# Kernel optimization log

Measured on AMD Instinct MI355X. Metric: run time of the kernel, lower is better.

The kernel has to match this reference:

```python
import jax, jax.numpy as jnp
import numpy as np

BATCH, IN, HID, OMID, OUT = 8192, 64, 1024, 128, 1
MAX_ITER = 8
EPS = 1e-3


def setup_inputs() -> dict:
    key = jax.random.key(0)
    ks = jax.random.split(key, 32)
    s_in, s_h = 1.0 / np.sqrt(IN), 1.0 / np.sqrt(HID)
    d = {"x": jax.random.normal(ks[0], (BATCH, IN), jnp.float32)}
    names = ["i", "f", "c", "o"]
    for j, n in enumerate(names):
        d[f"Wx{n}"] = jax.random.uniform(ks[1 + 4 * j], (HID, IN), jnp.float32, -s_in, s_in)
        d[f"bx{n}"] = jax.random.uniform(ks[2 + 4 * j], (HID,), jnp.float32, -s_in, s_in)
        d[f"Wh{n}"] = jax.random.uniform(ks[3 + 4 * j], (HID, HID), jnp.float32, -s_h, s_h)
        d[f"bh{n}"] = jax.random.uniform(ks[4 + 4 * j], (HID,), jnp.float32, -s_h, s_h)
    d["W_halt"] = jax.random.uniform(ks[20], (1, HID), jnp.float32, -s_h, s_h)
    d["b_halt"] = jax.random.uniform(ks[21], (1,), jnp.float32, -s_h, s_h)
    d["W1"] = jax.random.uniform(ks[22], (OMID, HID), jnp.float32, -s_h, s_h)
    d["b1"] = jax.random.uniform(ks[23], (OMID,), jnp.float32, -s_h, s_h)
    s_m = 1.0 / np.sqrt(OMID)
    d["W2"] = jax.random.uniform(ks[24], (OUT, OMID), jnp.float32, -s_m, s_m)
    d["b2"] = jax.random.uniform(ks[25], (OUT,), jnp.float32, -s_m, s_m)
    return d


def _act_forward(x, Wxi, bxi, Whi, bhi, Wxf, bxf, Whf, bhf, Wxc, bxc, Whc, bhc,
                 Wxo, bxo, Who, bho, W_halt, b_halt, W1, b1, W2, b2):
    B = x.shape[0]
    state0 = jnp.zeros((B, HID), x.dtype)
    cell0 = jnp.zeros((B, HID), x.dtype)
    p0 = jnp.zeros((B,), x.dtype)
    active0 = jnp.ones((B,), bool)

    def step(carry, t):
        state, cell, p_sum, active = carry
        # four LSTM-style gates (computed dense; masked update == torch's gather/scatter)
        i_g = jax.nn.sigmoid(x @ Wxi.T + bxi + state @ Whi.T + bhi)
        f_g = jax.nn.sigmoid(x @ Wxf.T + bxf + state @ Whf.T + bhf)
        c_g = jnp.tanh(x @ Wxc.T + bxc + state @ Whc.T + bhc)
        o_g = jax.nn.sigmoid(x @ Wxo.T + bxo + state @ Who.T + bho)
        am = active[:, None]
        cell = jnp.where(am, f_g * cell + i_g * c_g, cell)
        state = jnp.where(am, o_g * jnp.tanh(cell), state)
        out = jax.nn.sigmoid(jax.nn.relu(state @ W1.T + b1) @ W2.T + b2)  # (B, OUT)
        h = jax.nn.sigmoid(state @ W_halt.T + b_halt)[:, 0]               # (B,)
        p_new = p_sum + h
        last = t == MAX_ITER - 1
        finished = active & ((p_new >= 1.0 - EPS) | last)
        halt_rec = jnp.where(finished, 1.0 - p_sum, jnp.where(active, h, 0.0))
        p_sum = jnp.where(finished, 1.0, jnp.where(active, p_new, p_sum))
        out_rec = jnp.where(am, out, 0.0)
        active = active & ~finished
        return (state, cell, p_sum, active), (out_rec, halt_rec)

    _, (outs, halts) = jax.lax.scan(step, (state0, cell0, p0, active0), jnp.arange(MAX_ITER))
    # outs: (T, B, OUT), halts: (T, B); final = sum_t out_t * p_halt_t
    return jnp.einsum("tbo,tb->bo", outs, halts)


def reference(x, Wxi, bxi, Whi, bhi, Wxf, bxf, Whf, bhf, Wxc, bxc, Whc, bhc,
              Wxo, bxo, Who, bho, W_halt, b_halt, W1, b1, W2, b2):
    return _act_forward(x, Wxi, bxi, Whi, bhi, Wxf, bxf, Whf, bhf, Wxc, bxc, Whc, bhc,
                        Wxo, bxo, Who, bho, W_halt, b_halt, W1, b1, W2, b2)
```

## Files before the change

kernel.cpp:

```cpp
#include <hip/hip_runtime.h>
#include <hip/hip_bf16.h>

#define BATCH 8192
#define IN_DIM 64
#define HID 1024
#define KTOT 1088
#define NGATES 4096
#define OMID 128
#define NP 256
#define MAX_ITER 8

#define TM 128
#define TN 128
#define TK 64
#define TAILB 64

typedef __attribute__((ext_vector_type(8))) short short8;
typedef __attribute__((ext_vector_type(4))) float float4v;

__device__ __forceinline__ float bf2f(short s) {
    union { float f; unsigned u; } v; v.u = ((unsigned)(unsigned short)s) << 16; return v.f;
}
__device__ __forceinline__ short f2bf(float f) {
    union { float f; unsigned u; } v; v.f = f;
    unsigned r = v.u + 0x7fff + ((v.u >> 16) & 1);
    return (short)(r >> 16);
}
__device__ __forceinline__ float sigmoidf_(float x) {
    float xc = fminf(fmaxf(x, -30.f), 30.f);
    return 1.f / (1.f + __expf(-xc));
}
__device__ __forceinline__ float tanhf_(float x) {
    float xc = fminf(fmaxf(x, -15.f), 15.f);
    float e = __expf(2.f * xc);
    return (e - 1.f) / (e + 1.f);
}
__device__ __forceinline__ int aload(const int* p) {
    return __hip_atomic_load((int*)p, __ATOMIC_RELAXED, __HIP_MEMORY_SCOPE_AGENT);
}
__device__ __forceinline__ void astore(int* p, int v) {
    __hip_atomic_store(p, v, __ATOMIC_RELAXED, __HIP_MEMORY_SCOPE_AGENT);
}

__device__ __forceinline__ void gbar(int* bar, int phase, int tid) {
    __syncthreads();
    if (tid == 0) {
        __threadfence();
        __hip_atomic_fetch_add(bar, 1, __ATOMIC_ACQ_REL, __HIP_MEMORY_SCOPE_AGENT);
        while (aload(bar) < TAILB * phase)
            __builtin_amdgcn_s_sleep(8);
        __threadfence();
    }
    __syncthreads();
}

__device__ __forceinline__ void gates_tile(
    short* As, short* Bs, int tid,
    const short* __restrict__ A, const short* __restrict__ B,
    const float* __restrict__ bias_g, int K,
    float* __restrict__ cell, short* __restrict__ Aout,
    const int* __restrict__ ridx, int n_act, int m0, int bx)
{
    const int wave = tid >> 6, lane = tid & 63;
    const int wm = wave & 1, wn = wave >> 1;
    const int colq = lane & 15, q = lane >> 4;
    const int lrow8 = lane >> 3;
    const int lk    = (((lane & 7) ^ lrow8) * 8);
    const int n0 = bx * TN;

    int aoff[4][2], boff[4][2];
#pragma unroll
    for (int i = 0; i < 4; ++i) {
        const int Ra = wm * 64 + i * 16 + colq;
        const int Rb = wn * 64 + i * 16 + colq;
#pragma unroll
        for (int c2 = 0; c2 < 2; ++c2) {
            const int C = q + 4 * c2;
            aoff[i][c2] = Ra * TK + ((C ^ (Ra & 7)) << 3);
            boff[i][c2] = Rb * TK + ((C ^ (Rb & 7)) << 3);
        }
    }

    float4v acc[4][4];
#pragma unroll
    for (int i = 0; i < 4; ++i)
#pragma unroll
        for (int j = 0; j < 4; ++j) acc[i][j] = (float4v)0.f;

    const short* ga[4];
    const short* gb[4];
#pragma unroll
    for (int it = 0; it < 4; ++it) {
        const int rr = (wave * 4 + it) * 8;
        ga[it] = A + (size_t)ridx[m0 + rr + lrow8] * KTOT + lk;
        gb[it] = B + (size_t)(n0 + rr + lrow8) * KTOT + lk;
    }

    for (int k0 = 0; k0 < K; k0 += TK) {
#pragma unroll
        for (int it = 0; it < 4; ++it) {
            const int rr = (wave * 4 + it) * 8;
            __builtin_amdgcn_global_load_lds(
                (const __attribute__((address_space(1))) void*)ga[it],
                (__attribute__((address_space(3))) void*)(As + rr * TK), 16, 0, 0);
            __builtin_amdgcn_global_load_lds(
                (const __attribute__((address_space(1))) void*)gb[it],
                (__attribute__((address_space(3))) void*)(Bs + rr * TK), 16, 0, 0);
            ga[it] += TK; gb[it] += TK;
        }
        __syncthreads();
#pragma unroll
        for (int c2 = 0; c2 < 2; ++c2) {
            short8 af[4], bf[4];
#pragma unroll
            for (int i = 0; i < 4; ++i) {
                af[i] = *(const short8*)(As + aoff[i][c2]);
                bf[i] = *(const short8*)(Bs + boff[i][c2]);
            }
#pragma unroll
            for (int i = 0; i < 4; ++i)
#pragma unroll
                for (int j = 0; j < 4; ++j)
                    acc[i][j] = __builtin_amdgcn_mfma_f32_16x16x32_bf16(af[i], bf[j], acc[i][j], 0, 0, 0);
        }
        __syncthreads();
    }

    const int G = bx * 2 + wn;
    const int h = G * 16 + colq;
    const float bi  = bias_g[G * 64 +  0 + colq];
    const float bff = bias_g[G * 64 + 16 + colq];
    const float bc  = bias_g[G * 64 + 32 + colq];
    const float bo  = bias_g[G * 64 + 48 + colq];
#pragma unroll
    for (int i = 0; i < 4; ++i) {
        const int pbase = m0 + wm * 64 + i * 16 + q * 4;
#pragma unroll
        for (int r = 0; r < 4; ++r) {
            const int pos = pbase + r;
            if (pos < n_act) {
                const int row = ridx[pos];
                const float ig = sigmoidf_(acc[i][0][r] + bi);
                const float fg = sigmoidf_(acc[i][1][r] + bff);
                const float cg = tanhf_(acc[i][2][r] + bc);
                const float og = sigmoidf_(acc[i][3][r] + bo);
                const size_t ci = (size_t)row * HID + h;
                const float c = fg * cell[ci] + ig * cg;
                cell[ci] = c;
                Aout[(size_t)row * KTOT + h] = f2bf(og * tanhf_(c));
            }
        }
    }
    __syncthreads();
}

__device__ __forceinline__ void midfin_tile(
    short* As, short* Bs, int tid,
    const short* __restrict__ Anew, const short* __restrict__ P,
    const float* __restrict__ bias_p, const float* __restrict__ W_halt,
    const float* __restrict__ W2, const float* __restrict__ b2,
    float* __restrict__ outp, float* __restrict__ p_sum,
    const int* __restrict__ rprev, int* __restrict__ rnext,
    int* __restrict__ cnt, int t, int m0, int n_act)
{
    const int wave = tid >> 6, lane = tid & 63;
    const int wm = wave & 1, wn = wave >> 1;
    const int colq = lane & 15, q = lane >> 4;
    const int lrow8 = lane >> 3;
    const int lk    = (((lane & 7) ^ lrow8) * 8);

    float4v acc[4][4];
#pragma unroll
    for (int i = 0; i < 4; ++i)
#pragma unroll
        for (int j = 0; j < 4; ++j) acc[i][j] = (float4v)0.f;

    const short* ga[4];
    const short* gb[4];
#pragma unroll
    for (int it = 0; it < 4; ++it) {
        const int rr = (wave * 4 + it) * 8;
        ga[it] = Anew + (size_t)rprev[m0 + rr + lrow8] * KTOT + lk;
        gb[it] = P + (size_t)(rr + lrow8) * HID + lk;
    }
    int aoff[4][2], boff[4][2];
#pragma unroll
    for (int i = 0; i < 4; ++i) {
        const int Ra = wm * 64 + i * 16 + colq;
        const int Rb = wn * 64 + i * 16 + colq;
#pragma unroll
        for (int c2 = 0; c2 < 2; ++c2) {
            const int C = q + 4 * c2;
            aoff[i][c2] = Ra * TK + ((C ^ (Ra & 7)) << 3);
            boff[i][c2] = Rb * TK + ((C ^ (Rb & 7)) << 3);
        }
    }

    for (int k0 = 0; k0 < HID; k0 += TK) {
#pragma unroll
        for (int it = 0; it < 4; ++it) {
            const int rr = (wave * 4 + it) * 8;
            __builtin_amdgcn_global_load_lds(
                (const __attribute__((address_space(1))) void*)ga[it],
                (__attribute__((address_space(3))) void*)(As + rr * TK), 16, 0, 0);
            __builtin_amdgcn_global_load_lds(
                (const __attribute__((address_space(1))) void*)gb[it],
                (__attribute__((address_space(3))) void*)(Bs + rr * TK), 16, 0, 0);
            ga[it] += TK; gb[it] += TK;
        }
        __syncthreads();
#pragma unroll
        for (int c2 = 0; c2 < 2; ++c2) {
            short8 af[4], bf[4];
#pragma unroll
            for (int i = 0; i < 4; ++i) {
                af[i] = *(const short8*)(As + aoff[i][c2]);
                bf[i] = *(const short8*)(Bs + boff[i][c2]);
            }
#pragma unroll
            for (int i = 0; i < 4; ++i)
#pragma unroll
                for (int j = 0; j < 4; ++j)
                    acc[i][j] = __builtin_amdgcn_mfma_f32_16x16x32_bf16(af[i], bf[j], acc[i][j], 0, 0, 0);
        }
        __syncthreads();
    }

    float* red  = (float*)As;
    float* hbuf = ((float*)As) + 256;

    for (int s = 0; s < 32; ++s) {
        const int lr = wave * 32 + s;
        const int row = rprev[m0 + lr];
        const short* Ar = Anew + (size_t)row * KTOT + lane * 16;
        const short8 v0 = *(const short8*)Ar;
        const short8 v1 = *(const short8*)(Ar + 8);
        const float* Wh = W_halt + lane * 16;
        float hv = 0.f;
#pragma unroll
        for (int e = 0; e < 8; ++e) hv += bf2f(v0[e]) * Wh[e];
#pragma unroll
        for (int e = 0; e < 8; ++e) hv += bf2f(v1[e]) * Wh[8 + e];
#pragma unroll
        for (int o = 32; o > 0; o >>= 1) hv += __shfl_down(hv, o);
        if (lane == 0) hbuf[lr] = hv;
    }

    float pr[4][4];
#pragma unroll
    for (int i = 0; i < 4; ++i)
#pragma unroll
        for (int r = 0; r < 4; ++r) pr[i][r] = 0.f;
#pragma unroll
    for (int j = 0; j < 4; ++j) {
        const int col = wn * 64 + j * 16 + colq;
        const float b = bias_p[col];
        const float w2 = W2[col];
#pragma unroll
        for (int i = 0; i < 4; ++i)
#pragma unroll
            for (int r = 0; r < 4; ++r)
                pr[i][r] += fmaxf(acc[i][j][r] + b, 0.f) * w2;
    }
#pragma unroll
    for (int i = 0; i < 4; ++i)
#pragma unroll
        for (int r = 0; r < 4; ++r) {
            float v = pr[i][r];
            v += __shfl_down(v, 8, 16);
            v += __shfl_down(v, 4, 16);
            v += __shfl_down(v, 2, 16);
            v += __shfl_down(v, 1, 16);
            if (colq == 0)
                red[((((wn * 2) + wm) * 4 + i) * 4 + q) * 4 + r] = v;
        }
    __syncthreads();

    if (tid < TM) {
        const int pos = m0 + tid;
        if (pos < n_act) {
            const int lwm = tid >> 6, i = (tid >> 4) & 3, lq = (tid >> 2) & 3, r = tid & 3;
            const float odot = red[((lwm * 4 + i) * 4 + lq) * 4 + r]
                             + red[(((2 + lwm) * 4 + i) * 4 + lq) * 4 + r];
            const int row = rprev[pos];
            const float ov = sigmoidf_(odot + b2[0]);
            const float h  = sigmoidf_(hbuf[tid] + bias_p[OMID]);
            const float ps = p_sum[row];
            const float pn = ps + h;
            const bool fin = (pn >= 1.f - 1e-3f) || (t == MAX_ITER - 1);
            const float halt = fin ? (1.f - ps) : h;
            outp[row] += ov * halt;
            p_sum[row] = fin ? 1.f : pn;
            if (!fin) {
                const int d = atomicAdd(&cnt[t + 1], 1);
                astore(&rnext[d], row);
            }
        }
    }
    __syncthreads();
}

__global__ __launch_bounds__(256) void gates_k(
    const short* __restrict__ A, const short* __restrict__ B,
    const float* __restrict__ bias_g, int K,
    float* __restrict__ cell, short* __restrict__ Aout,
    const int* __restrict__ ridx, const int* __restrict__ cnt, int t)
{
    __shared__ short As[TM * TK];
    __shared__ short Bs[TN * TK];
    const int n_act = cnt[t];
    for (int by = blockIdx.y; by * TM < n_act; by += gridDim.y)
        gates_tile(As, Bs, threadIdx.x, A, B, bias_g, K, cell, Aout,
                   ridx, n_act, by * TM, blockIdx.x);
}

__global__ __launch_bounds__(256) void midfin_k(
    const short* __restrict__ Anew, const short* __restrict__ P,
    const float* __restrict__ bias_p, const float* __restrict__ W_halt,
    const float* __restrict__ W2, const float* __restrict__ b2,
    float* __restrict__ outp, float* __restrict__ p_sum,
    const int* __restrict__ rprev, int* __restrict__ rnext,
    int* __restrict__ cnt, int t)
{
    __shared__ short As[TM * TK];
    __shared__ short Bs[TN * TK];
    const int n_act = cnt[t];
    for (int tile = blockIdx.x; tile * TM < n_act; tile += gridDim.x)
        midfin_tile(As, Bs, threadIdx.x, Anew, P, bias_p, W_halt, W2, b2,
                    outp, p_sum, rprev, rnext, cnt, t, tile * TM, n_act);
}

__global__ __launch_bounds__(256) void tail_k(
    const short* __restrict__ Wg, const float* __restrict__ bias_g,
    const short* __restrict__ P, const float* __restrict__ bias_p,
    const float* __restrict__ W_halt, const float* __restrict__ W2,
    const float* __restrict__ b2,
    short* __restrict__ A0, short* __restrict__ A1,
    float* __restrict__ cell, float* __restrict__ outp,
    float* __restrict__ p_sum,
    int* __restrict__ ridx0, int* __restrict__ ridx1,
    int* __restrict__ cnt, int* __restrict__ bar)
{
    __shared__ short As[TM * TK];
    __shared__ short Bs[TN * TK];
    const int tid = threadIdx.x;
    int phase = 0;
    int t = 2;
    while (true) {
        short* Anew = (t & 1) ? A0 : A1;
        const int* rprev = (t & 1) ? ridx1 : ridx0;
        int* rnext = (t & 1) ? ridx0 : ridx1;
        const int n = aload(&cnt[t]);
        for (int tile = blockIdx.x; tile * TM < n; tile += gridDim.x)
            midfin_tile(As, Bs, tid, Anew, P, bias_p, W_halt, W2, b2,
                        outp, p_sum, rprev, rnext, cnt, t, tile * TM, n);
        if (t == MAX_ITER - 1) break;
        ++phase; gbar(bar, phase, tid);
        const int n1 = aload(&cnt[t + 1]);
        if (n1 == 0) break;
        {
            short* Aot = (t & 1) ? A1 : A0;
            const int ntiles = ((n1 + TM - 1) / TM) * (NGATES / TN);
            for (int e = blockIdx.x; e < ntiles; e += gridDim.x)
                gates_tile(As, Bs, tid, Anew, Wg, bias_g, KTOT, cell, Aot,
                           rnext, n1, (e >> 5) * TM, e & 31);
        }
        ++phase; gbar(bar, phase, tid);
        ++t;
    }
}

#define SETUP_INIT  (BATCH * KTOT)
#define SETUP_WG    (NGATES * KTOT)
#define SETUP_P     (NP * HID)
#define SETUP_TOT   (SETUP_INIT + SETUP_WG + SETUP_P)
__global__ __launch_bounds__(256) void setup_k(
    const float* __restrict__ x,
    const float* __restrict__ Whi, const float* __restrict__ Whf,
    const float* __restrict__ Whc, const float* __restrict__ Who,
    const float* __restrict__ Wxi, const float* __restrict__ Wxf,
    const float* __restrict__ Wxc, const float* __restrict__ Wxo,
    const float* __restrict__ bxi, const float* __restrict__ bhi,
    const float* __restrict__ bxf, const float* __restrict__ bhf,
    const float* __restrict__ bxc, const float* __restrict__ bhc,
    const float* __restrict__ bxo, const float* __restrict__ bho,
    const float* __restrict__ W1, const float* __restrict__ b1,
    const float* __restrict__ W_halt, const float* __restrict__ b_halt,
    short* __restrict__ A0, short* __restrict__ A1,
    float* __restrict__ cell, float* __restrict__ p_sum,
    int* __restrict__ ridx0, int* __restrict__ ridx1, int* __restrict__ cnt,
    int* __restrict__ bar, float* __restrict__ outp,
    short* __restrict__ Wg, float* __restrict__ bias_g,
    short* __restrict__ P, float* __restrict__ bias_p)
{
    int idx = blockIdx.x * 256 + threadIdx.x;
    if (idx < SETUP_INIT) {
        const int row = idx / KTOT, k = idx - row * KTOT;
        const short v = (k < HID) ? (short)0 : f2bf(x[row * IN_DIM + (k - HID)]);
        A0[idx] = v;
        A1[idx] = v;
        if (k < HID) cell[(size_t)row * HID + k] = 0.f;
        if (k == 0) {
            p_sum[row] = 0.f;
            outp[row] = 0.f;
            ridx0[row] = row;
            ridx1[row] = 0;
        }
        if (row == 0 && k <= MAX_ITER) cnt[k] = (k == 0) ? BATCH : 0;
        if (row == 1 && k == 0) bar[0] = 0;
        return;
    }
    idx -= SETUP_INIT;
    if (idx < SETUP_WG) {
        const int n = idx / KTOT, k = idx - n * KTOT;
        const int G = n >> 6, g = (n >> 4) & 3, q = n & 15;
        const int h = G * 16 + q;
        const float* Wh = (g == 0) ? Whi : (g == 1) ? Whf : (g == 2) ? Whc : Who;
        const float* Wx = (g == 0) ? Wxi : (g == 1) ? Wxf : (g == 2) ? Wxc : Wxo;
        const float v = (k < HID) ? Wh[h * HID + k] : Wx[h * IN_DIM + (k - HID)];
        Wg[idx] = f2bf(v);
        if (k == 0) {
            const float* bx = (g == 0) ? bxi : (g == 1) ? bxf : (g == 2) ? bxc : bxo;
            const float* bh = (g == 0) ? bhi : (g == 1) ? bhf : (g == 2) ? bhc : bho;
            bias_g[n] = bx[h] + bh[h];
        }
        return;
    }
    idx -= SETUP_WG;
    if (idx < SETUP_P) {
        const int n = idx >> 10, k = idx & 1023;
        const float v = (n < OMID) ? W1[n * HID + k] : (n == OMID ? W_halt[k] : 0.f);
        P[idx] = f2bf(v);
        if (k == 0) bias_p[n] = (n < OMID) ? b1[n] : (n == OMID ? b_halt[0] : 0.f);
    }
}

extern "C" void kernel_launch(void* const* d_in, const int* in_sizes, int n_in,
                              void* d_out, int out_size, void* d_ws, size_t ws_size,
                              hipStream_t stream) {
    const float* x    = (const float*)d_in[0];
    const float* Wxi  = (const float*)d_in[1];
    const float* bxi  = (const float*)d_in[2];
    const float* Whi  = (const float*)d_in[3];
    const float* bhi  = (const float*)d_in[4];
    const float* Wxf  = (const float*)d_in[5];
    const float* bxf  = (const float*)d_in[6];
    const float* Whf  = (const float*)d_in[7];
    const float* bhf  = (const float*)d_in[8];
    const float* Wxc  = (const float*)d_in[9];
    const float* bxc  = (const float*)d_in[10];
    const float* Whc  = (const float*)d_in[11];
    const float* bhc  = (const float*)d_in[12];
    const float* Wxo  = (const float*)d_in[13];
    const float* bxo  = (const float*)d_in[14];
    const float* Who  = (const float*)d_in[15];
    const float* bho  = (const float*)d_in[16];
    const float* W_halt = (const float*)d_in[17];
    const float* b_halt = (const float*)d_in[18];
    const float* W1   = (const float*)d_in[19];
    const float* b1   = (const float*)d_in[20];
    const float* W2   = (const float*)d_in[21];
    const float* b2   = (const float*)d_in[22];

    char* p = (char*)d_ws;
    auto carve = [&](size_t bytes) { char* r = p; p += (bytes + 255) & ~(size_t)255; return r; };
    short* A0     = (short*)carve((size_t)BATCH * KTOT * 2);
    short* A1     = (short*)carve((size_t)BATCH * KTOT * 2);
    short* Wg     = (short*)carve((size_t)NGATES * KTOT * 2);
    float* bias_g = (float*)carve((size_t)NGATES * 4);
    short* P      = (short*)carve((size_t)NP * HID * 2);
    float* bias_p = (float*)carve((size_t)NP * 4);
    float* cell   = (float*)carve((size_t)BATCH * HID * 4);
    float* p_sum  = (float*)carve((size_t)BATCH * 4);
    int*   ridx0  = (int*)carve((size_t)BATCH * 4);
    int*   ridx1  = (int*)carve((size_t)BATCH * 4);
    int*   cnt    = (int*)carve((size_t)(MAX_ITER + 1) * 4);
    int*   bar    = (int*)carve(256);
    float* outp   = (float*)d_out;

    setup_k<<<(SETUP_TOT + 255) / 256, 256, 0, stream>>>(
        x, Whi, Whf, Whc, Who, Wxi, Wxf, Wxc, Wxo,
        bxi, bhi, bxf, bhf, bxc, bhc, bxo, bho,
        W1, b1, W_halt, b_halt,
        A0, A1, cell, p_sum, ridx0, ridx1, cnt, bar, outp,
        Wg, bias_g, P, bias_p);

    gates_k<<<dim3(NGATES / TN, 32), 256, 0, stream>>>(
        A0 + HID, Wg + HID, bias_g, IN_DIM, cell, A1, ridx0, cnt, 0);
    midfin_k<<<64, 256, 0, stream>>>(
        A1, P, bias_p, W_halt, W2, b2, outp, p_sum, ridx0, ridx1, cnt, 0);
    gates_k<<<dim3(NGATES / TN, 32), 256, 0, stream>>>(
        A1, Wg, bias_g, KTOT, cell, A0, ridx1, cnt, 1);
    midfin_k<<<64, 256, 0, stream>>>(
        A0, P, bias_p, W_halt, W2, b2, outp, p_sum, ridx1, ridx0, cnt, 1);
    gates_k<<<dim3(NGATES / TN, 32), 256, 0, stream>>>(
        A0, Wg, bias_g, KTOT, cell, A1, ridx0, cnt, 2);
    tail_k<<<TAILB, 256, 0, stream>>>(
        Wg, bias_g, P, bias_p, W_halt, W2, b2,
        A0, A1, cell, outp, p_sum, ridx0, ridx1, cnt, bar);
}
```

Baseline: 496.4 us.

## Load gate GEMM operands directly from global memory into registers, bypassing LDS

The gates GEMM tile no longer stages A and B tiles through shared memory with global_load_lds and two barriers per K step. Each wave now loads its MFMA fragments straight from global memory (L2/L1), and the trailing block barrier is dropped. This removes LDS traffic and synchronisation, but each tile's data is fetched redundantly by several waves, and the per-lane loads are strided rather than coalesced. That can raise cache and memory pressure.

Measured after the change: 730.2 us. 47.1% more time.

```diff
diff --git a/kernel.cpp b/kernel.cpp
--- a/kernel.cpp
+++ b/kernel.cpp
@@ -55,8 +55,9 @@
 }
 
 __device__ __forceinline__ void gates_tile(
-    short* As, short* Bs, int tid,
-    const short* __restrict__ A, const short* __restrict__ B,
+    int tid,
+    const short* __restrict__ A,
+    const short* __restrict__ B,
     const float* __restrict__ bias_g, int K,
     float* __restrict__ cell, short* __restrict__ Aout,
     const int* __restrict__ ridx, int n_act, int m0, int bx)
@@ -64,21 +65,13 @@
     const int wave = tid >> 6, lane = tid & 63;
     const int wm = wave & 1, wn = wave >> 1;
     const int colq = lane & 15, q = lane >> 4;
-    const int lrow8 = lane >> 3;
-    const int lk    = (((lane & 7) ^ lrow8) * 8);
-    const int n0 = bx * TN;
-
-    int aoff[4][2], boff[4][2];
+
+    const short* pa[4];
+    const short* pb[4];
 #pragma unroll
     for (int i = 0; i < 4; ++i) {
-        const int Ra = wm * 64 + i * 16 + colq;
-        const int Rb = wn * 64 + i * 16 + colq;
-#pragma unroll
-        for (int c2 = 0; c2 < 2; ++c2) {
-            const int C = q + 4 * c2;
-            aoff[i][c2] = Ra * TK + ((C ^ (Ra & 7)) << 3);
-            boff[i][c2] = Rb * TK + ((C ^ (Rb & 7)) << 3);
-        }
+        pa[i] = A + (size_t)ridx[m0 + wm * 64 + i * 16 + colq] * KTOT + q * 8;
+        pb[i] = B + (size_t)(bx * TN + wn * 64 + i * 16 + colq) * KTOT + q * 8;
     }
 
     float4v acc[4][4];
@@ -87,43 +80,17 @@
 #pragma unroll
         for (int j = 0; j < 4; ++j) acc[i][j] = (float4v)0.f;
 
-    const short* ga[4];
-    const short* gb[4];
-#pragma unroll
-    for (int it = 0; it < 4; ++it) {
-        const int rr = (wave * 4 + it) * 8;
-        ga[it] = A + (size_t)ridx[m0 + rr + lrow8] * KTOT + lk;
-        gb[it] = B + (size_t)(n0 + rr + lrow8) * KTOT + lk;
-    }
-
-    for (int k0 = 0; k0 < K; k0 += TK) {
-#pragma unroll
-        for (int it = 0; it < 4; ++it) {
-            const int rr = (wave * 4 + it) * 8;
-            __builtin_amdgcn_global_load_lds(
-                (const __attribute__((address_space(1))) void*)ga[it],
-                (__attribute__((address_space(3))) void*)(As + rr * TK), 16, 0, 0);
-            __builtin_amdgcn_global_load_lds(
-                (const __attribute__((address_space(1))) void*)gb[it],
-                (__attribute__((address_space(3))) void*)(Bs + rr * TK), 16, 0, 0);
-            ga[it] += TK; gb[it] += TK;
-        }
-        __syncthreads();
-#pragma unroll
-        for (int c2 = 0; c2 < 2; ++c2) {
-            short8 af[4], bf[4];
-#pragma unroll
-            for (int i = 0; i < 4; ++i) {
-                af[i] = *(const short8*)(As + aoff[i][c2]);
-                bf[i] = *(const short8*)(Bs + boff[i][c2]);
-            }
-#pragma unroll
-            for (int i = 0; i < 4; ++i)
-#pragma unroll
-                for (int j = 0; j < 4; ++j)
-                    acc[i][j] = __builtin_amdgcn_mfma_f32_16x16x32_bf16(af[i], bf[j], acc[i][j], 0, 0, 0);
-        }
-        __syncthreads();
+    for (int k0 = 0; k0 < K; k0 += 32) {
+        short8 af[4], bf[4];
+#pragma unroll
+        for (int i = 0; i < 4; ++i) af[i] = *(const short8*)(pa[i] + k0);
+#pragma unroll
+        for (int j = 0; j < 4; ++j) bf[j] = *(const short8*)(pb[j] + k0);
+#pragma unroll
+        for (int i = 0; i < 4; ++i)
+#pragma unroll
+            for (int j = 0; j < 4; ++j)
+                acc[i][j] = __builtin_amdgcn_mfma_f32_16x16x32_bf16(af[i], bf[j], acc[i][j], 0, 0, 0);
     }
 
     const int G = bx * 2 + wn;
@@ -151,7 +118,6 @@
             }
         }
     }
-    __syncthreads();
 }
 
 __device__ __forceinline__ void midfin_tile(
@@ -306,11 +272,9 @@
     float* __restrict__ cell, short* __restrict__ Aout,
     const int* __restrict__ ridx, const int* __restrict__ cnt, int t)
 {
-    __shared__ short As[TM * TK];
-    __shared__ short Bs[TN * TK];
     const int n_act = cnt[t];
     for (int by = blockIdx.y; by * TM < n_act; by += gridDim.y)
-        gates_tile(As, Bs, threadIdx.x, A, B, bias_g, K, cell, Aout,
+        gates_tile(threadIdx.x, A, B, bias_g, K, cell, Aout,
                    ridx, n_act, by * TM, blockIdx.x);
 }
 
@@ -362,7 +326,7 @@
             short* Aot = (t & 1) ? A1 : A0;
             const int ntiles = ((n1 + TM - 1) / TM) * (NGATES / TN);
             for (int e = blockIdx.x; e < ntiles; e += gridDim.x)
-                gates_tile(As, Bs, tid, Anew, Wg, bias_g, KTOT, cell, Aot,
+                gates_tile(tid, Anew, Wg, bias_g, KTOT, cell, Aot,
                            rnext, n1, (e >> 5) * TM, e & 31);
         }
         ++phase; gbar(bar, phase, tid);
```

## Compute two M tiles per gates block to reuse each loaded B tile

Applied to the files above, without the earlier changes.

The gates GEMM kernel now has each block process two 128-row M tiles at once, sharing one loaded weight (B) tile between them, and the grid's y dimension is halved to match. This doubles the MFMA work per B load and cuts weight traffic through LDS and from global memory. In exchange the kernel needs twice the accumulator registers and more LDS, which limits it to 2 blocks per CU via launch bounds. When the second tile is inactive, its LDS buffer is still read, so it does wasted work on stale data. The old gates_tile is kept for the tail kernel.

New measurement: 457.7 us. -7.8%, faster.

```diff
diff --git a/kernel.cpp b/kernel.cpp
--- a/kernel.cpp
+++ b/kernel.cpp
@@ -13,6 +13,7 @@
 #define TM 128
 #define TN 128
 #define TK 64
+#define GYD 16
 #define TAILB 64
 
 typedef __attribute__((ext_vector_type(8))) short short8;
@@ -54,78 +55,13 @@
     __syncthreads();
 }
 
-__device__ __forceinline__ void gates_tile(
-    short* As, short* Bs, int tid,
-    const short* __restrict__ A, const short* __restrict__ B,
-    const float* __restrict__ bias_g, int K,
-    float* __restrict__ cell, short* __restrict__ Aout,
-    const int* __restrict__ ridx, int n_act, int m0, int bx)
-{
-    const int wave = tid >> 6, lane = tid & 63;
+__device__ __forceinline__ void gates_epilogue(
+    const float4v (&acc)[4][4], int m0, int bx, int wave, int lane,
+    const float* __restrict__ bias_g, float* __restrict__ cell,
+    short* __restrict__ Aout, const int* __restrict__ ridx, int n_act)
+{
     const int wm = wave & 1, wn = wave >> 1;
     const int colq = lane & 15, q = lane >> 4;
-    const int lrow8 = lane >> 3;
-    const int lk    = (((lane & 7) ^ lrow8) * 8);
-    const int n0 = bx * TN;
-
-    int aoff[4][2], boff[4][2];
-#pragma unroll
-    for (int i = 0; i < 4; ++i) {
-        const int Ra = wm * 64 + i * 16 + colq;
-        const int Rb = wn * 64 + i * 16 + colq;
-#pragma unroll
-        for (int c2 = 0; c2 < 2; ++c2) {
-            const int C = q + 4 * c2;
-            aoff[i][c2] = Ra * TK + ((C ^ (Ra & 7)) << 3);
-            boff[i][c2] = Rb * TK + ((C ^ (Rb & 7)) << 3);
-        }
-    }
-
-    float4v acc[4][4];
-#pragma unroll
-    for (int i = 0; i < 4; ++i)
-#pragma unroll
-        for (int j = 0; j < 4; ++j) acc[i][j] = (float4v)0.f;
-
-    const short* ga[4];
-    const short* gb[4];
-#pragma unroll
-    for (int it = 0; it < 4; ++it) {
-        const int rr = (wave * 4 + it) * 8;
-        ga[it] = A + (size_t)ridx[m0 + rr + lrow8] * KTOT + lk;
-        gb[it] = B + (size_t)(n0 + rr + lrow8) * KTOT + lk;
-    }
-
-    for (int k0 = 0; k0 < K; k0 += TK) {
-#pragma unroll
-        for (int it = 0; it < 4; ++it) {
-            const int rr = (wave * 4 + it) * 8;
-            __builtin_amdgcn_global_load_lds(
-                (const __attribute__((address_space(1))) void*)ga[it],
-                (__attribute__((address_space(3))) void*)(As + rr * TK), 16, 0, 0);
-            __builtin_amdgcn_global_load_lds(
-                (const __attribute__((address_space(1))) void*)gb[it],
-                (__attribute__((address_space(3))) void*)(Bs + rr * TK), 16, 0, 0);
-            ga[it] += TK; gb[it] += TK;
-        }
-        __syncthreads();
-#pragma unroll
-        for (int c2 = 0; c2 < 2; ++c2) {
-            short8 af[4], bf[4];
-#pragma unroll
-            for (int i = 0; i < 4; ++i) {
-                af[i] = *(const short8*)(As + aoff[i][c2]);
-                bf[i] = *(const short8*)(Bs + boff[i][c2]);
-            }
-#pragma unroll
-            for (int i = 0; i < 4; ++i)
-#pragma unroll
-                for (int j = 0; j < 4; ++j)
-                    acc[i][j] = __builtin_amdgcn_mfma_f32_16x16x32_bf16(af[i], bf[j], acc[i][j], 0, 0, 0);
-        }
-        __syncthreads();
-    }
-
     const int G = bx * 2 + wn;
     const int h = G * 16 + colq;
     const float bi  = bias_g[G * 64 +  0 + colq];
@@ -151,6 +87,178 @@
             }
         }
     }
+}
+
+__global__ __launch_bounds__(256, 2) void gates_k(
+    const short* __restrict__ A, const short* __restrict__ B,
+    const float* __restrict__ bias_g, int K,
+    float* __restrict__ cell, short* __restrict__ Aout,
+    const int* __restrict__ ridx, const int* __restrict__ cnt, int t)
+{
+    __shared__ short Bs[TN * TK];
+    __shared__ short As0[TM * TK];
+    __shared__ short As1[TM * TK];
+    const int n_act = cnt[t];
+    const int tid  = threadIdx.x;
+    const int wave = tid >> 6, lane = tid & 63;
+    const int wm = wave & 1, wn = wave >> 1;
+    const int colq = lane & 15, q = lane >> 4;
+    const int lrow8 = lane >> 3;
+    const int lk    = (((lane & 7) ^ lrow8) * 8);
+    const int n0 = blockIdx.x * TN;
+
+    int aoff[4][2], boff[4][2];
+#pragma unroll
+    for (int i = 0; i < 4; ++i) {
+        const int Ra = wm * 64 + i * 16 + colq;
+        const int Rb = wn * 64 + i * 16 + colq;
+#pragma unroll
+        for (int c2 = 0; c2 < 2; ++c2) {
+            const int C = q + 4 * c2;
+            aoff[i][c2] = Ra * TK + ((C ^ (Ra & 7)) << 3);
+            boff[i][c2] = Rb * TK + ((C ^ (Rb & 7)) << 3);
+        }
+    }
+
+    for (int by0 = blockIdx.y; by0 * TM < n_act; by0 += 2 * (int)gridDim.y) {
+        const int by1 = by0 + gridDim.y;
+        const bool dual = (by1 * TM < n_act);
+        const int m0 = by0 * TM, m1 = by1 * TM;
+
+        float4v acc0[4][4], acc1[4][4];
+#pragma unroll
+        for (int i = 0; i < 4; ++i)
+#pragma unroll
+            for (int j = 0; j < 4; ++j) { acc0[i][j] = (float4v)0.f; acc1[i][j] = (float4v)0.f; }
+
+        const short* ga0[4];
+        const short* ga1[4];
+        const short* gb[4];
+#pragma unroll
+        for (int it = 0; it < 4; ++it) {
+            const int rr = (wave * 4 + it) * 8;
+            ga0[it] = A + (size_t)ridx[m0 + rr + lrow8] * KTOT + lk;
+            ga1[it] = dual ? A + (size_t)ridx[m1 + rr + lrow8] * KTOT + lk : ga0[it];
+            gb[it]  = B + (size_t)(n0 + rr + lrow8) * KTOT + lk;
+        }
+
+        for (int k0 = 0; k0 < K; k0 += TK) {
+#pragma unroll
+            for (int it = 0; it < 4; ++it) {
+                const int rr = (wave * 4 + it) * 8;
+                __builtin_amdgcn_global_load_lds(
+                    (const __attribute__((address_space(1))) void*)gb[it],
+                    (__attribute__((address_space(3))) void*)(Bs + rr * TK), 16, 0, 0);
+                __builtin_amdgcn_global_load_lds(
+                    (const __attribute__((address_space(1))) void*)ga0[it],
+                    (__attribute__((address_space(3))) void*)(As0 + rr * TK), 16, 0, 0);
+                if (dual)
+                    __builtin_amdgcn_global_load_lds(
+                        (const __attribute__((address_space(1))) void*)ga1[it],
+                        (__attribute__((address_space(3))) void*)(As1 + rr * TK), 16, 0, 0);
+                ga0[it] += TK; ga1[it] += TK; gb[it] += TK;
+            }
+            __syncthreads();
+#pragma unroll
+            for (int c2 = 0; c2 < 2; ++c2) {
+                short8 bf[4], af0[4], af1[4];
+#pragma unroll
+                for (int i = 0; i < 4; ++i) {
+                    bf[i]  = *(const short8*)(Bs  + boff[i][c2]);
+                    af0[i] = *(const short8*)(As0 + aoff[i][c2]);
+                    af1[i] = *(const short8*)(As1 + aoff[i][c2]);
+                }
+#pragma unroll
+                for (int i = 0; i < 4; ++i)
+#pragma unroll
+                    for (int j = 0; j < 4; ++j) {
+                        acc0[i][j] = __builtin_amdgcn_mfma_f32_16x16x32_bf16(af0[i], bf[j], acc0[i][j], 0, 0, 0);
+                        acc1[i][j] = __builtin_amdgcn_mfma_f32_16x16x32_bf16(af1[i], bf[j], acc1[i][j], 0, 0, 0);
+                    }
+            }
+            __syncthreads();
+        }
+
+        gates_epilogue(acc0, m0, blockIdx.x, wave, lane, bias_g, cell, Aout, ridx, n_act);
+        if (dual)
+            gates_epilogue(acc1, m1, blockIdx.x, wave, lane, bias_g, cell, Aout, ridx, n_act);
+        __syncthreads();
+    }
+}
+
+__device__ __forceinline__ void gates_tile(
+    short* As, short* Bs, int tid,
+    const short* __restrict__ A, const short* __restrict__ B,
+    const float* __restrict__ bias_g, int K,
+    float* __restrict__ cell, short* __restrict__ Aout,
+    const int* __restrict__ ridx, int n_act, int m0, int bx)
+{
+    const int wave = tid >> 6, lane = tid & 63;
+    const int wm = wave & 1, wn = wave >> 1;
+    const int colq = lane & 15, q = lane >> 4;
+    const int lrow8 = lane >> 3;
+    const int lk    = (((lane & 7) ^ lrow8) * 8);
+    const int n0 = bx * TN;
+
+    int aoff[4][2], boff[4][2];
+#pragma unroll
+    for (int i = 0; i < 4; ++i) {
+        const int Ra = wm * 64 + i * 16 + colq;
+        const int Rb = wn * 64 + i * 16 + colq;
+#pragma unroll
+        for (int c2 = 0; c2 < 2; ++c2) {
+            const int C = q + 4 * c2;
+            aoff[i][c2] = Ra * TK + ((C ^ (Ra & 7)) << 3);
+            boff[i][c2] = Rb * TK + ((C ^ (Rb & 7)) << 3);
+        }
+    }
+
+    float4v acc[4][4];
+#pragma unroll
+    for (int i = 0; i < 4; ++i)
+#pragma unroll
+        for (int j = 0; j < 4; ++j) acc[i][j] = (float4v)0.f;
+
+    const short* ga[4];
+    const short* gb[4];
+#pragma unroll
+    for (int it = 0; it < 4; ++it) {
+        const int rr = (wave * 4 + it) * 8;
+        ga[it] = A + (size_t)ridx[m0 + rr + lrow8] * KTOT + lk;
+        gb[it] = B + (size_t)(n0 + rr + lrow8) * KTOT + lk;
+    }
+
+    for (int k0 = 0; k0 < K; k0 += TK) {
+#pragma unroll
+        for (int it = 0; it < 4; ++it) {
+            const int rr = (wave * 4 + it) * 8;
+            __builtin_amdgcn_global_load_lds(
+                (const __attribute__((address_space(1))) void*)ga[it],
+                (__attribute__((address_space(3))) void*)(As + rr * TK), 16, 0, 0);
+            __builtin_amdgcn_global_load_lds(
+                (const __attribute__((address_space(1))) void*)gb[it],
+                (__attribute__((address_space(3))) void*)(Bs + rr * TK), 16, 0, 0);
+            ga[it] += TK; gb[it] += TK;
+        }
+        __syncthreads();
+#pragma unroll
+        for (int c2 = 0; c2 < 2; ++c2) {
+            short8 af[4], bf[4];
+#pragma unroll
+            for (int i = 0; i < 4; ++i) {
+                af[i] = *(const short8*)(As + aoff[i][c2]);
+                bf[i] = *(const short8*)(Bs + boff[i][c2]);
+            }
+#pragma unroll
+            for (int i = 0; i < 4; ++i)
+#pragma unroll
+                for (int j = 0; j < 4; ++j)
+                    acc[i][j] = __builtin_amdgcn_mfma_f32_16x16x32_bf16(af[i], bf[j], acc[i][j], 0, 0, 0);
+        }
+        __syncthreads();
+    }
+
+    gates_epilogue(acc, m0, bx, wave, lane, bias_g, cell, Aout, ridx, n_act);
     __syncthreads();
 }
 
@@ -298,20 +406,6 @@
         }
     }
     __syncthreads();
-}
-
-__global__ __launch_bounds__(256) void gates_k(
-    const short* __restrict__ A, const short* __restrict__ B,
-    const float* __restrict__ bias_g, int K,
-    float* __restrict__ cell, short* __restrict__ Aout,
-    const int* __restrict__ ridx, const int* __restrict__ cnt, int t)
-{
-    __shared__ short As[TM * TK];
-    __shared__ short Bs[TN * TK];
-    const int n_act = cnt[t];
-    for (int by = blockIdx.y; by * TM < n_act; by += gridDim.y)
-        gates_tile(As, Bs, threadIdx.x, A, B, bias_g, K, cell, Aout,
-                   ridx, n_act, by * TM, blockIdx.x);
 }
 
 __global__ __launch_bounds__(256) void midfin_k(
@@ -485,15 +579,15 @@
         A0, A1, cell, p_sum, ridx0, ridx1, cnt, bar, outp,
         Wg, bias_g, P, bias_p);
 
-    gates_k<<<dim3(NGATES / TN, 32), 256, 0, stream>>>(
+    gates_k<<<dim3(NGATES / TN, GYD), 256, 0, stream>>>(
         A0 + HID, Wg + HID, bias_g, IN_DIM, cell, A1, ridx0, cnt, 0);
     midfin_k<<<64, 256, 0, stream>>>(
         A1, P, bias_p, W_halt, W2, b2, outp, p_sum, ridx0, ridx1, cnt, 0);
-    gates_k<<<dim3(NGATES / TN, 32), 256, 0, stream>>>(
+    gates_k<<<dim3(NGATES / TN, GYD), 256, 0, stream>>>(
         A1, Wg, bias_g, KTOT, cell, A0, ridx1, cnt, 1);
     midfin_k<<<64, 256, 0, stream>>>(
         A0, P, bias_p, W_halt, W2, b2, outp, p_sum, ridx1, ridx0, cnt, 1);
-    gates_k<<<dim3(NGATES / TN, 32), 256, 0, stream>>>(
+    gates_k<<<dim3(NGATES / TN, GYD), 256, 0, stream>>>(
         A0, Wg, bias_g, KTOT, cell, A1, ridx0, cnt, 2);
     tail_k<<<TAILB, 256, 0, stream>>>(
         Wg, bias_g, P, bias_p, W_halt, W2, b2,
```
